# Performance work log

Hardware: AMD Instinct MI355X
Metric: run time of the kernel (lower is better)

## Reference

```python
import jax, jax.numpy as jnp
import numpy as np
from jax.scipy.special import digamma, polygamma

N_ITERS = 100
TOL = 1e-3


def setup_inputs() -> dict:
    key = jax.random.key(0)
    x = jax.random.normal(key, (2_000_000, 10), dtype=jnp.float32)
    return {"x": x}


def reference(x):
    # x: [n, C] logits -> Dirichlet MLE over softmax probabilities
    p = jax.nn.softmax(x, axis=-1)            # [n, C]
    n = p.shape[0]
    m1 = p.mean(0)                            # [C] E[p]
    m2 = (p ** 2).mean(0)                     # [C] E[p^2]
    # method-of-moments initialization (as in the torch module)
    a0 = m1 * ((m1 - m2) / (m2 - m1 ** 2)).mean(-1)
    # loop-invariant sufficient statistic
    log_p_avg = jnp.log(p).mean(0)            # [C]

    def cond(carry):
        a, k, diff = carry
        return jnp.logical_and(k < N_ITERS, diff >= TOL)

    def body(carry):
        a, k, _ = carry
        g = (digamma(a.sum(-1)) - digamma(a) + log_p_avg) * n
        q = -n * polygamma(1, a)
        z = n * polygamma(1, a.sum(-1))
        q_inv = 1.0 / q
        b = (g * q_inv).sum(-1) / (1.0 / z + q_inv.sum(-1))
        a_new = a - (g - b) / q               # Newton step with rank-1 Hessian inverse
        diff = jnp.abs(a_new - a).sum()       # L1 norm, matches torch.norm(.,1)
        return (a_new, k + 1, diff)

    a, _, _ = jax.lax.while_loop(
        cond, body, (a0, jnp.int32(0), jnp.float32(jnp.inf))
    )
    return a.astype(jnp.float32)
```

## Files before the change

kernel.cpp:

```cpp
#include <hip/hip_runtime.h>
#include <math.h>

#define C 10
#define BLOCK 256
#define NBLOCKS 1024
#define WROWS 128
#define WELEMS (WROWS * C)
#define NSTATS (3 * C)

typedef float f4 __attribute__((ext_vector_type(4)));


__device__ __forceinline__ void accum_row(const float* __restrict__ row,
                                          float* __restrict__ s1,
                                          float* __restrict__ s2,
                                          float* __restrict__ sl) {
  float v[C];
#pragma unroll
  for (int c = 0; c < C; c++) v[c] = row[c];
  float mx = v[0];
#pragma unroll
  for (int c = 1; c < C; c++) mx = fmaxf(mx, v[c]);
  float e[C], se = 0.f;
#pragma unroll
  for (int c = 0; c < C; c++) { v[c] -= mx; e[c] = __expf(v[c]); se += e[c]; }
  float inv = 1.0f / se;
  float lse = __logf(se);
#pragma unroll
  for (int c = 0; c < C; c++) {
    float p = e[c] * inv;
    s1[c] += p;
    s2[c] = fmaf(p, p, s2[c]);
    sl[c] += v[c] - lse;
  }
}


__global__ __launch_bounds__(BLOCK) void dir_stats_kernel(
    const float* __restrict__ x, float* __restrict__ partials,
    int nrows, int nblocks) {
  __shared__ float buf[4][2][WELEMS];
  __shared__ float red[4][NSTATS];
  const int tid = threadIdx.x;
  const int lane = tid & 63;
  const int wave = tid >> 6;

  const int gwave = blockIdx.x * 4 + wave;
  const int wstride = nblocks * 4;
  const int ntiles = nrows / WROWS;
  const int tailStart = ntiles * WROWS;

  float s1[C], s2[C], sl[C];
#pragma unroll
  for (int c = 0; c < C; c++) { s1[c] = 0.f; s2[c] = 0.f; sl[c] = 0.f; }

  int g = gwave;
  f4 a0 = 0, a1 = 0, a2 = 0, a3 = 0, a4 = 0;
  if (g < ntiles) {
    const f4* __restrict__ p = (const f4*)(x + (size_t)g * WELEMS) + lane;
    a0 = p[0]; a1 = p[64]; a2 = p[128]; a3 = p[192]; a4 = p[256];
  }
  int phase = 0;
  while (g < ntiles) {
    f4* dst = (f4*)buf[wave][phase] + lane;
    dst[0] = a0; dst[64] = a1; dst[128] = a2; dst[192] = a3; dst[256] = a4;

    const int gn = g + wstride;
    if (gn < ntiles) {
      const f4* __restrict__ p = (const f4*)(x + (size_t)gn * WELEMS) + lane;
      a0 = p[0]; a1 = p[64]; a2 = p[128]; a3 = p[192]; a4 = p[256];
    }

    accum_row(buf[wave][phase] + (size_t)lane * C, s1, s2, sl);
    accum_row(buf[wave][phase] + (size_t)(64 + lane) * C, s1, s2, sl);

    g = gn; phase ^= 1;
  }

  if (gwave == wstride - 1) {
    for (int rr = tailStart + lane; rr < nrows; rr += 64) {
      float v[C];
      const float* r = x + (size_t)rr * C;
#pragma unroll
      for (int c = 0; c < C; c++) v[c] = r[c];
      float mx = v[0];
#pragma unroll
      for (int c = 1; c < C; c++) mx = fmaxf(mx, v[c]);
      float e[C], se = 0.f;
#pragma unroll
      for (int c = 0; c < C; c++) { v[c] -= mx; e[c] = __expf(v[c]); se += e[c]; }
      float inv = 1.0f / se, lse = __logf(se);
#pragma unroll
      for (int c = 0; c < C; c++) {
        float p = e[c] * inv;
        s1[c] += p; s2[c] = fmaf(p, p, s2[c]); sl[c] += v[c] - lse;
      }
    }
  }

#pragma unroll
  for (int c = 0; c < C; c++) {
    float v1 = s1[c], v2 = s2[c], v3 = sl[c];
#pragma unroll
    for (int off = 32; off >= 1; off >>= 1) {
      v1 += __shfl_down(v1, off);
      v2 += __shfl_down(v2, off);
      v3 += __shfl_down(v3, off);
    }
    if (lane == 0) {
      red[wave][c] = v1;
      red[wave][C + c] = v2;
      red[wave][2 * C + c] = v3;
    }
  }
  __syncthreads();
  if (tid < NSTATS) {
    float tot = red[0][tid] + red[1][tid] + red[2][tid] + red[3][tid];
    partials[(size_t)tid * nblocks + blockIdx.x] = tot;
  }
}


__device__ __forceinline__ void digtri8(double x, double& dg, double& tg) {
  double i0 = 1.0 / x,         i1 = 1.0 / (x + 1.0);
  double i2 = 1.0 / (x + 2.0), i3 = 1.0 / (x + 3.0);
  double i4 = 1.0 / (x + 4.0), i5 = 1.0 / (x + 5.0);
  double i6 = 1.0 / (x + 6.0), i7 = 1.0 / (x + 7.0);
  double rd = (i0 + i1) + (i2 + i3) + ((i4 + i5) + (i6 + i7));
  double rt = (i0 * i0 + i1 * i1) + (i2 * i2 + i3 * i3) +
              ((i4 * i4 + i5 * i5) + (i6 * i6 + i7 * i7));
  double y = x + 8.0;
  double yi = 1.0 / y, f = yi * yi;
  dg = log(y) - 0.5 * yi
     - f * (1.0 / 12 - f * (1.0 / 120 - f * (1.0 / 252 - f * (1.0 / 240 - f * (1.0 / 132)))))
     - rd;
  tg = rt + yi + 0.5 * f
     + f * yi * (1.0 / 6 - f * (1.0 / 30 - f * (1.0 / 42 - f * (1.0 / 30))));
}

__device__ __forceinline__ double wsum16(double v) {
#pragma unroll
  for (int off = 1; off < 16; off <<= 1) v += __shfl_xor(v, off);
  return v;
}

__global__ __launch_bounds__(1024) void dir_newton_kernel(
    const float* __restrict__ partials, float* __restrict__ out,
    int nparts, double nrows) {
  __shared__ double tot[NSTATS];
  const int tid = threadIdx.x;

  {
    const int j = tid >> 5;
    const int k = tid & 31;
    double s = 0.0;
    if (j < NSTATS) {
      const float* __restrict__ base = partials + (size_t)j * nparts;
#pragma unroll 8
      for (int b = k; b < nparts; b += 32)
        s += (double)base[b];
    }
#pragma unroll
    for (int off = 16; off >= 1; off >>= 1) s += __shfl_xor(s, off);
    if (j < NSTATS && k == 0) tot[j] = s;
  }
  __syncthreads();

  if (tid < 16) {
    const int c = tid;
    const bool act = (c < C);
    const double n = nrows;
    double m1 = 0.0, m2 = 0.0, lpa = 0.0;
    if (act) {
      m1 = tot[c] / n;
      m2 = tot[C + c] / n;
      lpa = tot[2 * C + c] / n;
    }
    double ratio = act ? (m1 - m2) / (m2 - m1 * m1) : 0.0;
    double rmean = wsum16(ratio) / (double)C;
    double a = act ? m1 * rmean : 0.0;

    double diff = 1e30;
    for (int k = 0; k < 100 && diff >= 1e-3; k++) {
      double S = wsum16(a);
      double dgl, tgl;
      digtri8(act ? a : S, dgl, tgl);
      double dgS = __shfl(dgl, 10);
      double tgS = __shfl(tgl, 10);
      double g = act ? (dgS - dgl + lpa) * n : 0.0;
      double qinv = act ? (-1.0) / (n * tgl) : 0.0;
      double z = n * tgS;
      double num = wsum16(g * qinv);
      double den = 1.0 / z + wsum16(qinv);
      double b = num / den;
      double anew = act ? a - (g - b) * qinv : 0.0;
      diff = wsum16(fabs(anew - a));
      a = anew;
    }
    if (act) out[c] = (float)a;
  }
}


extern "C" void kernel_launch(void* const* d_in, const int* in_sizes, int n_in,
                              void* d_out, int out_size, void* d_ws, size_t ws_size,
                              hipStream_t stream) {
  const float* x = (const float*)d_in[0];
  const int total = in_sizes[0];
  const int nrows = total / C;

  int grid = NBLOCKS;
  size_t need = (size_t)NSTATS * grid * sizeof(float);
  if (need > ws_size) {
    grid = (int)(ws_size / (NSTATS * sizeof(float)));
    if (grid < 1) grid = 1;
  }

  float* partials = (float*)d_ws;
  dir_stats_kernel<<<grid, BLOCK, 0, stream>>>(x, partials, nrows, grid);
  dir_newton_kernel<<<1, 1024, 0, stream>>>(partials, (float*)d_out, grid, (double)nrows);
}
```

Baseline: 123.1 us.

## Fuse stats and Newton kernels via last-block atomic counter, use nontemporal loads

Merges the streaming statistics kernel and the single-block Newton solve into one launch. Each block publishes its partials, bumps an atomic counter, and the last block to finish reduces all partials and runs the Newton iterations. This removes the second kernel launch and its gap, at the cost of a memset before the kernel and a serial tail that runs on one 256-thread block instead of 1024 threads. Input loads also switch to nontemporal builtins to avoid polluting the cache with single-use data.

```diff
diff --git a/kernel.cpp b/kernel.cpp
--- a/kernel.cpp
+++ b/kernel.cpp
@@ -10,6 +10,8 @@
 
 typedef float f4 __attribute__((ext_vector_type(4)));
 
+#define NTL4(p) __builtin_nontemporal_load(p)
+
 
 __device__ __forceinline__ void accum_row(const float* __restrict__ row,
                                           float* __restrict__ s1,
@@ -32,91 +34,6 @@
     s1[c] += p;
     s2[c] = fmaf(p, p, s2[c]);
     sl[c] += v[c] - lse;
-  }
-}
-
-
-__global__ __launch_bounds__(BLOCK) void dir_stats_kernel(
-    const float* __restrict__ x, float* __restrict__ partials,
-    int nrows, int nblocks) {
-  __shared__ float buf[4][2][WELEMS];
-  __shared__ float red[4][NSTATS];
-  const int tid = threadIdx.x;
-  const int lane = tid & 63;
-  const int wave = tid >> 6;
-
-  const int gwave = blockIdx.x * 4 + wave;
-  const int wstride = nblocks * 4;
-  const int ntiles = nrows / WROWS;
-  const int tailStart = ntiles * WROWS;
-
-  float s1[C], s2[C], sl[C];
-#pragma unroll
-  for (int c = 0; c < C; c++) { s1[c] = 0.f; s2[c] = 0.f; sl[c] = 0.f; }
-
-  int g = gwave;
-  f4 a0 = 0, a1 = 0, a2 = 0, a3 = 0, a4 = 0;
-  if (g < ntiles) {
-    const f4* __restrict__ p = (const f4*)(x + (size_t)g * WELEMS) + lane;
-    a0 = p[0]; a1 = p[64]; a2 = p[128]; a3 = p[192]; a4 = p[256];
-  }
-  int phase = 0;
-  while (g < ntiles) {
-    f4* dst = (f4*)buf[wave][phase] + lane;
-    dst[0] = a0; dst[64] = a1; dst[128] = a2; dst[192] = a3; dst[256] = a4;
-
-    const int gn = g + wstride;
-    if (gn < ntiles) {
-      const f4* __restrict__ p = (const f4*)(x + (size_t)gn * WELEMS) + lane;
-      a0 = p[0]; a1 = p[64]; a2 = p[128]; a3 = p[192]; a4 = p[256];
-    }
-
-    accum_row(buf[wave][phase] + (size_t)lane * C, s1, s2, sl);
-    accum_row(buf[wave][phase] + (size_t)(64 + lane) * C, s1, s2, sl);
-
-    g = gn; phase ^= 1;
-  }
-
-  if (gwave == wstride - 1) {
-    for (int rr = tailStart + lane; rr < nrows; rr += 64) {
-      float v[C];
-      const float* r = x + (size_t)rr * C;
-#pragma unroll
-      for (int c = 0; c < C; c++) v[c] = r[c];
-      float mx = v[0];
-#pragma unroll
-      for (int c = 1; c < C; c++) mx = fmaxf(mx, v[c]);
-      float e[C], se = 0.f;
-#pragma unroll
-      for (int c = 0; c < C; c++) { v[c] -= mx; e[c] = __expf(v[c]); se += e[c]; }
-      float inv = 1.0f / se, lse = __logf(se);
-#pragma unroll
-      for (int c = 0; c < C; c++) {
-        float p = e[c] * inv;
-        s1[c] += p; s2[c] = fmaf(p, p, s2[c]); sl[c] += v[c] - lse;
-      }
-    }
-  }
-
-#pragma unroll
-  for (int c = 0; c < C; c++) {
-    float v1 = s1[c], v2 = s2[c], v3 = sl[c];
-#pragma unroll
-    for (int off = 32; off >= 1; off >>= 1) {
-      v1 += __shfl_down(v1, off);
-      v2 += __shfl_down(v2, off);
-      v3 += __shfl_down(v3, off);
-    }
-    if (lane == 0) {
-      red[wave][c] = v1;
-      red[wave][C + c] = v2;
-      red[wave][2 * C + c] = v3;
-    }
-  }
-  __syncthreads();
-  if (tid < NSTATS) {
-    float tot = red[0][tid] + red[1][tid] + red[2][tid] + red[3][tid];
-    partials[(size_t)tid * nblocks + blockIdx.x] = tot;
   }
 }
 
@@ -144,37 +61,129 @@
   return v;
 }
 
-__global__ __launch_bounds__(1024) void dir_newton_kernel(
-    const float* __restrict__ partials, float* __restrict__ out,
-    int nparts, double nrows) {
-  __shared__ double tot[NSTATS];
+
+__global__ __launch_bounds__(BLOCK) void dir_fused_kernel(
+    const float* __restrict__ x, float* __restrict__ out,
+    float* __restrict__ partials, unsigned int* __restrict__ ctr,
+    int nrows, int nblocks, double nd) {
+  __shared__ float buf[4][2][WELEMS];
+  __shared__ float red[4][NSTATS];
+  __shared__ double totd[32];
+  __shared__ int lastFlag;
+
   const int tid = threadIdx.x;
+  const int lane = tid & 63;
+  const int wave = tid >> 6;
+
+  const int gwave = blockIdx.x * 4 + wave;
+  const int wstride = nblocks * 4;
+  const int ntiles = nrows / WROWS;
+  const int tailStart = ntiles * WROWS;
+
+  float s1[C], s2[C], sl[C];
+#pragma unroll
+  for (int c = 0; c < C; c++) { s1[c] = 0.f; s2[c] = 0.f; sl[c] = 0.f; }
+
+  int g = gwave;
+  f4 a0 = 0, a1 = 0, a2 = 0, a3 = 0, a4 = 0;
+  if (g < ntiles) {
+    const f4* __restrict__ p = (const f4*)(x + (size_t)g * WELEMS) + lane;
+    a0 = NTL4(p); a1 = NTL4(p + 64); a2 = NTL4(p + 128);
+    a3 = NTL4(p + 192); a4 = NTL4(p + 256);
+  }
+  int phase = 0;
+  while (g < ntiles) {
+    f4* dst = (f4*)buf[wave][phase] + lane;
+    dst[0] = a0; dst[64] = a1; dst[128] = a2; dst[192] = a3; dst[256] = a4;
+
+    const int gn = g + wstride;
+    if (gn < ntiles) {
+      const f4* __restrict__ p = (const f4*)(x + (size_t)gn * WELEMS) + lane;
+      a0 = NTL4(p); a1 = NTL4(p + 64); a2 = NTL4(p + 128);
+      a3 = NTL4(p + 192); a4 = NTL4(p + 256);
+    }
+
+    accum_row(buf[wave][phase] + (size_t)lane * C, s1, s2, sl);
+    accum_row(buf[wave][phase] + (size_t)(64 + lane) * C, s1, s2, sl);
+
+    g = gn; phase ^= 1;
+  }
+
+  if (gwave == wstride - 1) {
+    for (int rr = tailStart + lane; rr < nrows; rr += 64) {
+      float v[C];
+      const float* r = x + (size_t)rr * C;
+#pragma unroll
+      for (int c = 0; c < C; c++) v[c] = r[c];
+      float mx = v[0];
+#pragma unroll
+      for (int c = 1; c < C; c++) mx = fmaxf(mx, v[c]);
+      float e[C], se = 0.f;
+#pragma unroll
+      for (int c = 0; c < C; c++) { v[c] -= mx; e[c] = __expf(v[c]); se += e[c]; }
+      float inv = 1.0f / se, lse = __logf(se);
+#pragma unroll
+      for (int c = 0; c < C; c++) {
+        float p = e[c] * inv;
+        s1[c] += p; s2[c] = fmaf(p, p, s2[c]); sl[c] += v[c] - lse;
+      }
+    }
+  }
+
+#pragma unroll
+  for (int c = 0; c < C; c++) {
+    float v1 = s1[c], v2 = s2[c], v3 = sl[c];
+#pragma unroll
+    for (int off = 32; off >= 1; off >>= 1) {
+      v1 += __shfl_down(v1, off);
+      v2 += __shfl_down(v2, off);
+      v3 += __shfl_down(v3, off);
+    }
+    if (lane == 0) {
+      red[wave][c] = v1;
+      red[wave][C + c] = v2;
+      red[wave][2 * C + c] = v3;
+    }
+  }
+  __syncthreads();
+  if (tid < NSTATS) {
+    float tot = red[0][tid] + red[1][tid] + red[2][tid] + red[3][tid];
+    partials[(size_t)tid * nblocks + blockIdx.x] = tot;
+  }
+
+  __threadfence();
+  __syncthreads();
+  if (tid == 0)
+    lastFlag = (atomicAdd(ctr, 1u) == (unsigned)(nblocks - 1));
+  __syncthreads();
+  if (!lastFlag) return;
+  __threadfence();
 
   {
-    const int j = tid >> 5;
-    const int k = tid & 31;
+    const int j = tid >> 3;
+    const int k = tid & 7;
     double s = 0.0;
     if (j < NSTATS) {
-      const float* __restrict__ base = partials + (size_t)j * nparts;
+      const float* __restrict__ base = partials + (size_t)j * nblocks;
 #pragma unroll 8
-      for (int b = k; b < nparts; b += 32)
-        s += (double)base[b];
-    }
-#pragma unroll
-    for (int off = 16; off >= 1; off >>= 1) s += __shfl_xor(s, off);
-    if (j < NSTATS && k == 0) tot[j] = s;
+      for (int b = k; b < nblocks; b += 8) s += (double)base[b];
+    }
+    s += __shfl_down(s, 4);
+    s += __shfl_down(s, 2);
+    s += __shfl_down(s, 1);
+    if (j < NSTATS && k == 0) totd[j] = s;
   }
   __syncthreads();
 
   if (tid < 16) {
     const int c = tid;
     const bool act = (c < C);
-    const double n = nrows;
+    const double n = nd;
     double m1 = 0.0, m2 = 0.0, lpa = 0.0;
     if (act) {
-      m1 = tot[c] / n;
-      m2 = tot[C + c] / n;
-      lpa = tot[2 * C + c] / n;
+      m1 = totd[c] / n;
+      m2 = totd[C + c] / n;
+      lpa = totd[2 * C + c] / n;
     }
     double ratio = act ? (m1 - m2) / (m2 - m1 * m1) : 0.0;
     double rmean = wsum16(ratio) / (double)C;
@@ -210,13 +219,16 @@
   const int nrows = total / C;
 
   int grid = NBLOCKS;
-  size_t need = (size_t)NSTATS * grid * sizeof(float);
+  size_t need = 64 + (size_t)NSTATS * grid * sizeof(float);
   if (need > ws_size) {
-    grid = (int)(ws_size / (NSTATS * sizeof(float)));
+    grid = (int)((ws_size - 64) / (NSTATS * sizeof(float)));
     if (grid < 1) grid = 1;
   }
 
-  float* partials = (float*)d_ws;
-  dir_stats_kernel<<<grid, BLOCK, 0, stream>>>(x, partials, nrows, grid);
-  dir_newton_kernel<<<1, 1024, 0, stream>>>(partials, (float*)d_out, grid, (double)nrows);
-}
+  unsigned int* ctr = (unsigned int*)d_ws;
+  float* partials = (float*)((char*)d_ws + 64);
+
+  hipMemsetAsync(d_ws, 0, sizeof(unsigned int), stream);
+  dir_fused_kernel<<<grid, BLOCK, 0, stream>>>(x, (float*)d_out, partials, ctr,
+                                               nrows, grid, (double)nrows);
+}
```

After: 211.3 us. 71.7% more time.
